# Kernel tuning notes

Hardware: AMD Instinct MI355X
Metric: run time of the kernel (lower is better)

## Reference

```python
import jax, jax.numpy as jnp
import numpy as np

BS, C_IN, H, W = 16, 128, 64, 64
C_OUT, K, STRIDE, PAD, DIL = 256, 3, 1, 1, 1
ALPHA = 0.5  # scaling_factor
QMAX = 127.0  # int8 symmetric fake-quant


def _fake_quant(t):
    # symmetric per-tensor int8 fake quantization with straight-through estimator
    s = jax.lax.stop_gradient(jnp.max(jnp.abs(t))) / QMAX
    s = jnp.where(s == 0, 1.0, s)
    q = jnp.clip(jnp.round(t / s), -QMAX, QMAX) * s
    return t + jax.lax.stop_gradient(q - t)  # STE


def setup_inputs() -> dict:
    key = jax.random.key(0)
    k1, k2, k3 = jax.random.split(key, 3)
    x = jax.random.normal(k1, (BS, C_IN, H, W), dtype=jnp.float32)
    weight = jax.random.normal(k2, (C_OUT, C_IN, K, K), dtype=jnp.float32) * 0.05
    bias = jax.random.normal(k3, (C_OUT,), dtype=jnp.float32) * 0.01
    return {"x": x, "weight": weight, "bias": bias}


def reference(x, weight, bias):
    bs, _, h_in, w_in = x.shape
    ickhkw = C_IN * K * K
    h_out = (h_in + 2 * PAD - DIL * (K - 1) - 1) // STRIDE + 1
    w_out = (w_in + 2 * PAD - DIL * (K - 1) - 1) // STRIDE + 1

    # im2col (matches torch F.unfold feature ordering: channel-major, then kh, kw)
    patches = jax.lax.conv_general_dilated_patches(
        x, filter_shape=(K, K), window_strides=(STRIDE, STRIDE),
        padding=((PAD, PAD), (PAD, PAD)), rhs_dilation=(DIL, DIL),
    )  # [bs, ickhkw, h_out, w_out]
    cols = patches.reshape(bs, ickhkw, h_out * w_out)
    cols = cols.transpose(0, 2, 1).reshape(-1, ickhkw)  # [bs*L, ickhkw]

    w2 = weight.reshape(C_OUT, ickhkw)

    # SmoothQuant per-column scales (detached)
    w_scale = jax.lax.stop_gradient(jnp.max(jnp.abs(w2), axis=0))    # [ickhkw]
    act_scale = jax.lax.stop_gradient(jnp.max(jnp.abs(cols), axis=0))  # [ickhkw]
    scale = act_scale ** ALPHA / w_scale ** (1.0 - ALPHA)
    scale = jnp.where(scale == 0, 1.0, scale)

    w_s = _fake_quant(w2 * scale)
    x_s = _fake_quant(cols / scale)

    out = x_s @ w_s.T  # [bs*L, C_OUT]
    out = out.reshape(bs, h_out * w_out, C_OUT).transpose(0, 2, 1)
    out = out.reshape(bs, C_OUT, h_out, w_out)
    return out + bias.reshape(1, C_OUT, 1, 1)
```

## Files before the change

### kernel.cpp

```cpp
#include <hip/hip_runtime.h>
#include <cstdint>

#define C_IN   128
#define C_OUT  256
#define KK     1152
#define NPIX   4096
#define BS     16
#define M_ROWS 65536
#define QMAXF  127.0f

typedef int v4i __attribute__((ext_vector_type(4)));

#define OFF_QW    75497472
#define OFF_SCALE 75792384
#define OFF_QMUL  75796992
#define OFF_APART 75801600
#define OFF_SCAL  75843072

__global__ void k_prep(const float* __restrict__ x, const float* __restrict__ wgt,
                       float* __restrict__ act_part, float* __restrict__ w_part) {
    const int tid = threadIdx.x;
    if (blockIdx.x >= 1024) {
        int t = blockIdx.x - 1024;
        int j = (t % 5) * 256 + tid;
        int s = t / 5;
        if (j >= KK) return;
        const float* p = wgt + (size_t)s * 16 * KK + j;
        float m = 0.f;
#pragma unroll
        for (int i = 0; i < 16; i++) m = fmaxf(m, fabsf(p[(size_t)i * KK]));
        w_part[s * KK + j] = m;
        return;
    }
    const int c = blockIdx.x >> 3, s = blockIdx.x & 7;
    float m[9];
#pragma unroll
    for (int i = 0; i < 9; i++) m[i] = 0.f;
    for (int p = tid; p < 2 * NPIX; p += 256) {
        int b = s * 2 + (p >> 12);
        int hw = p & 4095;
        int h = hw >> 6, w = hw & 63;
        float v = fabsf(x[b * (C_IN * NPIX) + c * NPIX + hw]);
        bool rr[3] = { h <= 62, true, h >= 1 };
        bool cc[3] = { w <= 62, true, w >= 1 };
#pragma unroll
        for (int i = 0; i < 3; i++)
#pragma unroll
            for (int jq = 0; jq < 3; jq++)
                m[i * 3 + jq] = fmaxf(m[i * 3 + jq], (rr[i] && cc[jq]) ? v : 0.f);
    }
    __shared__ float sm[9][4];
    int lane = tid & 63, wid = tid >> 6;
#pragma unroll
    for (int i = 0; i < 9; i++) {
        float v = m[i];
        for (int off = 32; off > 0; off >>= 1) v = fmaxf(v, __shfl_down(v, off));
        if (lane == 0) sm[i][wid] = v;
    }
    __syncthreads();
    if (tid < 9) {
        float v = fmaxf(fmaxf(sm[tid][0], sm[tid][1]), fmaxf(sm[tid][2], sm[tid][3]));
        act_part[s * KK + c * 9 + tid] = v;
    }
}

__global__ void k_scales(const float* __restrict__ act_part, const float* __restrict__ w_part,
                         float* __restrict__ scale, float* __restrict__ qmul,
                         float* __restrict__ scalars) {
    const int tid = threadIdx.x;
    float sc_local[2] = {1.f, 1.f};
    float mx = 0.f, mw = 0.f;
#pragma unroll
    for (int t = 0; t < 2; t++) {
        int j = tid + t * 1024;
        if (j < KK) {
            float a = 0.f;
#pragma unroll
            for (int s = 0; s < 8; s++) a = fmaxf(a, act_part[s * KK + j]);
            float wv = 0.f;
#pragma unroll
            for (int s = 0; s < 16; s++) wv = fmaxf(wv, w_part[s * KK + j]);
            float sc = sqrtf(a) / sqrtf(wv);
            if (sc == 0.f) sc = 1.0f;
            scale[j] = sc;
            sc_local[t] = sc;
            mx = fmaxf(mx, a / sc);
            mw = fmaxf(mw, wv * sc);
        }
    }
    __shared__ float smx[16], smw[16];
    __shared__ float s_x_sh;
    int lane = tid & 63, wid = tid >> 6;
    for (int off = 32; off > 0; off >>= 1) {
        mx = fmaxf(mx, __shfl_down(mx, off));
        mw = fmaxf(mw, __shfl_down(mw, off));
    }
    if (lane == 0) { smx[wid] = mx; smw[wid] = mw; }
    __syncthreads();
    if (tid == 0) {
        float a = 0.f, b = 0.f;
        for (int i = 0; i < 16; i++) { a = fmaxf(a, smx[i]); b = fmaxf(b, smw[i]); }
        float s_x = a / QMAXF; if (s_x == 0.f) s_x = 1.f;
        float s_w = b / QMAXF; if (s_w == 0.f) s_w = 1.f;
        scalars[0] = s_x; scalars[1] = s_w; scalars[2] = s_x * s_w;
        s_x_sh = s_x;
    }
    __syncthreads();
    float s_x = s_x_sh;
#pragma unroll
    for (int t = 0; t < 2; t++) {
        int j = tid + t * 1024;
        if (j < KK) qmul[j] = 1.0f / (sc_local[t] * s_x);
    }
}

__global__ void k_quant_w(const float* __restrict__ wgt, const float* __restrict__ scale,
                          const float* __restrict__ scalars, signed char* __restrict__ qWp) {
    int idx = blockIdx.x * 256 + threadIdx.x;
    int m  = (unsigned)idx / KK;
    int kp = idx - m * KK;
    int tap = kp >> 7, c = kp & 127;
    int j = c * 9 + tap;
    float s_w = scalars[1];
    float t = wgt[m * KK + j] * scale[j];
    float q = rintf(t / s_w);
    q = fminf(fmaxf(q, -QMAXF), QMAXF);
    qWp[idx] = (signed char)(int)q;
}

__global__ __launch_bounds__(512, 4) void k_gemm(const signed char* __restrict__ qWp,
                                                 const float* __restrict__ x,
                                                 const float* __restrict__ qmul,
                                                 const float* __restrict__ scalars,
                                                 const float* __restrict__ bias,
                                                 float* __restrict__ out) {
    __shared__ __align__(16) signed char Bs[2][64 * 128];
    __shared__ float qm[KK];
    const int tid = threadIdx.x;
    const int lane = tid & 63, wv = tid >> 6;
    const int bid = blockIdx.x;
    const int swz = (bid & 7) * 128 + (bid >> 3);
    const int b  = swz >> 6;
    const int oh = swz & 63;
    const float* xb = x + (size_t)b * (C_IN * NPIX);
    const int c0 = wv * 16;

    for (int i = tid; i < KK; i += 512) {
        int tap = i >> 7, c = i & 127;
        qm[i] = qmul[c * 9 + tap];
    }

    const signed char* aBase = qWp + (size_t)(wv * 32 + (lane & 15)) * KK + (lane >> 4) * 16;

    v4i acc[2][4];
#pragma unroll
    for (int i = 0; i < 2; i++)
#pragma unroll
        for (int jq = 0; jq < 4; jq++) acc[i][jq] = (v4i){0, 0, 0, 0};

    float xr[16], xrn[16];
    {
        const bool ok = oh >= 1;
        const float* s = xb + (oh - 1) * 64 + lane;
#pragma unroll
        for (int d = 0; d < 16; d++) xr[d] = ok ? s[(size_t)(c0 + d) * NPIX] : 0.f;
    }
    v4i af[2][2], afn[2][2];
#pragma unroll
    for (int h = 0; h < 2; h++)
#pragma unroll
        for (int mt = 0; mt < 2; mt++)
            af[h][mt] = *(const v4i*)(aBase + (size_t)mt * 16 * KK + 0 * 128 + h * 64);

    __syncthreads();

#pragma unroll
    for (int tap = 0; tap < 9; tap++) {
        const int g  = (tap * 11) >> 5;
        const int jj = tap - g * 3;
        const int s  = jj - 1;
        const bool rowok = ((unsigned)(oh - 1 + g)) < 64u;
        signed char* bsp = (signed char*)Bs[tap & 1];

        {
            int n = lane - s;
            bool valid = (unsigned)n < 64u;
            int wrow = valid ? n : (s == -1 ? 0 : 63);
            bool live = rowok && valid;
            const float* qmt = qm + tap * 128 + c0;
            int pk[4];
#pragma unroll
            for (int d4 = 0; d4 < 4; d4++) {
                int w = 0;
#pragma unroll
                for (int e = 0; e < 4; e++) {
                    float v = live ? xr[d4 * 4 + e] : 0.f;
                    float q = rintf(v * qmt[d4 * 4 + e]);
                    w |= ((int)q & 255) << (8 * e);
                }
                pk[d4] = w;
            }
            *(v4i*)(bsp + wrow * 128 + ((wv ^ (wrow & 7)) * 16)) = (v4i){pk[0], pk[1], pk[2], pk[3]};
        }

        if (jj == 0 && g < 2) {
            const bool ok = (unsigned)(oh + g) < 64u;
            const float* sp = xb + (oh + g) * 64 + lane;
#pragma unroll
            for (int d = 0; d < 16; d++) xrn[d] = ok ? sp[(size_t)(c0 + d) * NPIX] : 0.f;
        }

        __syncthreads();

        if (tap < 8) {
#pragma unroll
            for (int h = 0; h < 2; h++)
#pragma unroll
                for (int mt = 0; mt < 2; mt++)
                    afn[h][mt] = *(const v4i*)(aBase + (size_t)mt * 16 * KK + (tap + 1) * 128 + h * 64);
        }

#pragma unroll
        for (int h = 0; h < 2; h++) {
            const int q4 = h * 4 + (lane >> 4);
            v4i bf[4];
#pragma unroll
            for (int nt = 0; nt < 4; nt++) {
                int rb = nt * 16 + (lane & 15);
                bf[nt] = *(const v4i*)(bsp + rb * 128 + ((q4 ^ (rb & 7)) * 16));
            }
#pragma unroll
            for (int mt = 0; mt < 2; mt++)
#pragma unroll
                for (int nt = 0; nt < 4; nt++)
                    acc[mt][nt] = __builtin_amdgcn_mfma_i32_16x16x64_i8(af[h][mt], bf[nt], acc[mt][nt], 0, 0, 0);
        }

        if (tap < 8) {
#pragma unroll
            for (int h = 0; h < 2; h++)
#pragma unroll
                for (int mt = 0; mt < 2; mt++) af[h][mt] = afn[h][mt];
        }
        if (jj == 2 && g < 2) {
#pragma unroll
            for (int d = 0; d < 16; d++) xr[d] = xrn[d];
        }
    }

    const float ssp = scalars[2];
    const int quad = lane >> 4, col = lane & 15;
    float bv[2][4];
#pragma unroll
    for (int mt = 0; mt < 2; mt++)
#pragma unroll
        for (int rg = 0; rg < 4; rg++)
            bv[mt][rg] = bias[wv * 32 + mt * 16 + quad * 4 + rg];

    float* obase = out + ((size_t)b * C_OUT) * NPIX + oh * 64;
#pragma unroll
    for (int mt = 0; mt < 2; mt++) {
#pragma unroll
        for (int nt = 0; nt < 4; nt++) {
            int n = nt * 16 + col;
#pragma unroll
            for (int rg = 0; rg < 4; rg++) {
                int m = wv * 32 + mt * 16 + quad * 4 + rg;
                obase[(size_t)m * NPIX + n] = (float)acc[mt][nt][rg] * ssp + bv[mt][rg];
            }
        }
    }
}

extern "C" void kernel_launch(void* const* d_in, const int* in_sizes, int n_in,
                              void* d_out, int out_size, void* d_ws, size_t ws_size,
                              hipStream_t stream) {
    const float* x    = (const float*)d_in[0];
    const float* wgt  = (const float*)d_in[1];
    const float* bias = (const float*)d_in[2];
    float* out = (float*)d_out;

    char* ws = (char*)d_ws;
    signed char* qWp = (signed char*)(ws + OFF_QW);
    float* w_part    = (float*)(ws + OFF_QW);
    float* scale     = (float*)(ws + OFF_SCALE);
    float* qmul      = (float*)(ws + OFF_QMUL);
    float* act_part  = (float*)(ws + OFF_APART);
    float* scalars   = (float*)(ws + OFF_SCAL);

    k_prep<<<1104, 256, 0, stream>>>(x, wgt, act_part, w_part);
    k_scales<<<1, 1024, 0, stream>>>(act_part, w_part, scale, qmul, scalars);
    k_quant_w<<<(C_OUT * KK) / 256, 256, 0, stream>>>(wgt, scale, scalars, qWp);
    k_gemm<<<BS * 64, 512, 0, stream>>>(qWp, x, qmul, scalars, bias, out);
}
```

Baseline: 153.8 us.

## Vectorize act-max prep, fuse scale and weight-quant kernels, pack int8 with perm

The activation abs-max prep now reads float4 and derives the nine tap maxima from per-vector partial maxima. The scale computation and weight quantization are merged into one 257-block kernel in which every block recomputes the per-column scales into shared memory, removing a launch and the global scale buffer. The GEMM's B-tile quantization packs bytes with perm instructions and drops a redundant row-validity check. In exchange, the partial-max arrays are read redundantly by every block, and w_part moves to a separate workspace offset.

```diff
diff --git a/kernel.cpp b/kernel.cpp
--- a/kernel.cpp
+++ b/kernel.cpp
@@ -11,6 +11,7 @@
 
 typedef int v4i __attribute__((ext_vector_type(4)));
 
+#define OFF_WPART 0
 #define OFF_QW    75497472
 #define OFF_SCALE 75792384
 #define OFF_QMUL  75796992
@@ -36,18 +37,28 @@
     float m[9];
 #pragma unroll
     for (int i = 0; i < 9; i++) m[i] = 0.f;
-    for (int p = tid; p < 2 * NPIX; p += 256) {
-        int b = s * 2 + (p >> 12);
-        int hw = p & 4095;
-        int h = hw >> 6, w = hw & 63;
-        float v = fabsf(x[b * (C_IN * NPIX) + c * NPIX + hw]);
-        bool rr[3] = { h <= 62, true, h >= 1 };
-        bool cc[3] = { w <= 62, true, w >= 1 };
-#pragma unroll
-        for (int i = 0; i < 3; i++)
-#pragma unroll
-            for (int jq = 0; jq < 3; jq++)
-                m[i * 3 + jq] = fmaxf(m[i * 3 + jq], (rr[i] && cc[jq]) ? v : 0.f);
+    const float4* xp4 = (const float4*)(x + (size_t)(s * 2) * (C_IN * NPIX) + (size_t)c * NPIX);
+    const int img4 = C_IN * NPIX / 4;
+    for (int v = tid; v < 2048; v += 256) {
+        int half = v >> 10;
+        int hw4  = v & 1023;
+        int h   = hw4 >> 4;
+        int w4i = hw4 & 15;
+        float4 f = xp4[half * img4 + hw4];
+        float ax = fabsf(f.x), ay = fabsf(f.y), az = fabsf(f.z), aw = fabsf(f.w);
+        float vall = fmaxf(fmaxf(ax, ay), fmaxf(az, aw));
+        float vnoF = (w4i == 0)  ? fmaxf(fmaxf(ay, az), aw) : vall;
+        float vnoL = (w4i == 15) ? fmaxf(fmaxf(ax, ay), az) : vall;
+        bool r0 = (h <= 62), r2 = (h >= 1);
+        m[0] = fmaxf(m[0], r0 ? vnoL : 0.f);
+        m[1] = fmaxf(m[1], r0 ? vall : 0.f);
+        m[2] = fmaxf(m[2], r0 ? vnoF : 0.f);
+        m[3] = fmaxf(m[3], vnoL);
+        m[4] = fmaxf(m[4], vall);
+        m[5] = fmaxf(m[5], vnoF);
+        m[6] = fmaxf(m[6], r2 ? vnoL : 0.f);
+        m[7] = fmaxf(m[7], r2 ? vall : 0.f);
+        m[8] = fmaxf(m[8], r2 ? vnoF : 0.f);
     }
     __shared__ float sm[9][4];
     int lane = tid & 63, wid = tid >> 6;
@@ -64,68 +75,60 @@
     }
 }
 
-__global__ void k_scales(const float* __restrict__ act_part, const float* __restrict__ w_part,
-                         float* __restrict__ scale, float* __restrict__ qmul,
-                         float* __restrict__ scalars) {
+__global__ void k_scalequant(const float* __restrict__ act_part, const float* __restrict__ w_part,
+                             const float* __restrict__ wgt,
+                             float* __restrict__ qmul, float* __restrict__ scalars,
+                             signed char* __restrict__ qWp) {
     const int tid = threadIdx.x;
-    float sc_local[2] = {1.f, 1.f};
+    __shared__ float ssc[KK];
+    __shared__ float red[16];
+    __shared__ float s_sw, s_sx;
     float mx = 0.f, mw = 0.f;
-#pragma unroll
-    for (int t = 0; t < 2; t++) {
-        int j = tid + t * 1024;
-        if (j < KK) {
-            float a = 0.f;
-#pragma unroll
-            for (int s = 0; s < 8; s++) a = fmaxf(a, act_part[s * KK + j]);
-            float wv = 0.f;
-#pragma unroll
-            for (int s = 0; s < 16; s++) wv = fmaxf(wv, w_part[s * KK + j]);
-            float sc = sqrtf(a) / sqrtf(wv);
-            if (sc == 0.f) sc = 1.0f;
-            scale[j] = sc;
-            sc_local[t] = sc;
-            mx = fmaxf(mx, a / sc);
-            mw = fmaxf(mw, wv * sc);
-        }
-    }
-    __shared__ float smx[16], smw[16];
-    __shared__ float s_x_sh;
+    for (int j = tid; j < KK; j += 256) {
+        float a = 0.f;
+#pragma unroll
+        for (int s = 0; s < 8; s++) a = fmaxf(a, act_part[s * KK + j]);
+        float wv = 0.f;
+#pragma unroll
+        for (int s = 0; s < 16; s++) wv = fmaxf(wv, w_part[s * KK + j]);
+        float sc = sqrtf(a) / sqrtf(wv);
+        if (sc == 0.f) sc = 1.0f;
+        ssc[j] = sc;
+        mx = fmaxf(mx, a / sc);
+        mw = fmaxf(mw, wv * sc);
+    }
     int lane = tid & 63, wid = tid >> 6;
     for (int off = 32; off > 0; off >>= 1) {
         mx = fmaxf(mx, __shfl_down(mx, off));
         mw = fmaxf(mw, __shfl_down(mw, off));
     }
-    if (lane == 0) { smx[wid] = mx; smw[wid] = mw; }
+    if (lane == 0) { red[wid] = mx; red[8 + wid] = mw; }
     __syncthreads();
     if (tid == 0) {
-        float a = 0.f, b = 0.f;
-        for (int i = 0; i < 16; i++) { a = fmaxf(a, smx[i]); b = fmaxf(b, smw[i]); }
+        float a = fmaxf(fmaxf(red[0], red[1]), fmaxf(red[2], red[3]));
+        float b = fmaxf(fmaxf(red[8], red[9]), fmaxf(red[10], red[11]));
         float s_x = a / QMAXF; if (s_x == 0.f) s_x = 1.f;
         float s_w = b / QMAXF; if (s_w == 0.f) s_w = 1.f;
-        scalars[0] = s_x; scalars[1] = s_w; scalars[2] = s_x * s_w;
-        s_x_sh = s_x;
-    }
-    __syncthreads();
-    float s_x = s_x_sh;
-#pragma unroll
-    for (int t = 0; t < 2; t++) {
-        int j = tid + t * 1024;
-        if (j < KK) qmul[j] = 1.0f / (sc_local[t] * s_x);
-    }
-}
-
-__global__ void k_quant_w(const float* __restrict__ wgt, const float* __restrict__ scale,
-                          const float* __restrict__ scalars, signed char* __restrict__ qWp) {
-    int idx = blockIdx.x * 256 + threadIdx.x;
-    int m  = (unsigned)idx / KK;
-    int kp = idx - m * KK;
-    int tap = kp >> 7, c = kp & 127;
-    int j = c * 9 + tap;
-    float s_w = scalars[1];
-    float t = wgt[m * KK + j] * scale[j];
-    float q = rintf(t / s_w);
-    q = fminf(fmaxf(q, -QMAXF), QMAXF);
-    qWp[idx] = (signed char)(int)q;
+        s_sx = s_x; s_sw = s_w;
+    }
+    __syncthreads();
+    const int bid = blockIdx.x;
+    if (bid == 0) {
+        const float s_x = s_sx, s_w = s_sw;
+        if (tid == 0) { scalars[0] = s_x; scalars[1] = s_w; scalars[2] = s_x * s_w; }
+        for (int j = tid; j < KK; j += 256) qmul[j] = 1.0f / (ssc[j] * s_x);
+        return;
+    }
+    const int m = bid - 1;
+    const float s_w = s_sw;
+    for (int kp = tid; kp < KK; kp += 256) {
+        int tap = kp >> 7, c = kp & 127;
+        int j = c * 9 + tap;
+        float t = wgt[(size_t)m * KK + j] * ssc[j];
+        float q = rintf(t / s_w);
+        q = fminf(fmaxf(q, -QMAXF), QMAXF);
+        qWp[(size_t)m * KK + kp] = (signed char)(int)q;
+    }
 }
 
 __global__ __launch_bounds__(512, 4) void k_gemm(const signed char* __restrict__ qWp,
@@ -179,26 +182,24 @@
         const int g  = (tap * 11) >> 5;
         const int jj = tap - g * 3;
         const int s  = jj - 1;
-        const bool rowok = ((unsigned)(oh - 1 + g)) < 64u;
         signed char* bsp = (signed char*)Bs[tap & 1];
 
         {
             int n = lane - s;
             bool valid = (unsigned)n < 64u;
             int wrow = valid ? n : (s == -1 ? 0 : 63);
-            bool live = rowok && valid;
             const float* qmt = qm + tap * 128 + c0;
             int pk[4];
 #pragma unroll
             for (int d4 = 0; d4 < 4; d4++) {
-                int w = 0;
-#pragma unroll
-                for (int e = 0; e < 4; e++) {
-                    float v = live ? xr[d4 * 4 + e] : 0.f;
-                    float q = rintf(v * qmt[d4 * 4 + e]);
-                    w |= ((int)q & 255) << (8 * e);
-                }
-                pk[d4] = w;
+                int q0 = (int)rintf(xr[d4 * 4 + 0] * qmt[d4 * 4 + 0]);
+                int q1 = (int)rintf(xr[d4 * 4 + 1] * qmt[d4 * 4 + 1]);
+                int q2 = (int)rintf(xr[d4 * 4 + 2] * qmt[d4 * 4 + 2]);
+                int q3 = (int)rintf(xr[d4 * 4 + 3] * qmt[d4 * 4 + 3]);
+                unsigned t0 = __builtin_amdgcn_perm((unsigned)q1, (unsigned)q0, 0x0c0c0400u);
+                unsigned t1 = __builtin_amdgcn_perm((unsigned)q3, (unsigned)q2, 0x0c0c0400u);
+                int w = (int)__builtin_amdgcn_perm(t1, t0, 0x05040100u);
+                pk[d4] = valid ? w : 0;
             }
             *(v4i*)(bsp + wrow * 128 + ((wv ^ (wrow & 7)) * 16)) = (v4i){pk[0], pk[1], pk[2], pk[3]};
         }
@@ -281,15 +282,13 @@
     float* out = (float*)d_out;
 
     char* ws = (char*)d_ws;
+    float* w_part    = (float*)(ws + OFF_WPART);
     signed char* qWp = (signed char*)(ws + OFF_QW);
-    float* w_part    = (float*)(ws + OFF_QW);
-    float* scale     = (float*)(ws + OFF_SCALE);
     float* qmul      = (float*)(ws + OFF_QMUL);
     float* act_part  = (float*)(ws + OFF_APART);
     float* scalars   = (float*)(ws + OFF_SCAL);
 
     k_prep<<<1104, 256, 0, stream>>>(x, wgt, act_part, w_part);
-    k_scales<<<1, 1024, 0, stream>>>(act_part, w_part, scale, qmul, scalars);
-    k_quant_w<<<(C_OUT * KK) / 256, 256, 0, stream>>>(wgt, scale, scalars, qWp);
+    k_scalequant<<<257, 256, 0, stream>>>(act_part, w_part, wgt, qmul, scalars, qWp);
     k_gemm<<<BS * 64, 512, 0, stream>>>(qWp, x, qmul, scalars, bias, out);
 }
```

Result: faster. 142.6 us (-7.3%).
